# Performance work log

Measured on AMD Instinct MI355X. Metric: run time of the kernel, lower is better.

The kernel has to match this reference:

```python
import jax, jax.numpy as jnp
import numpy as np

B, P, ENC = 32, 196, 2048
E, H, A, V, T = 512, 512, 512, 10000, 21
S = 0.02  # param init scale


def setup_inputs() -> dict:
    key = jax.random.key(0)
    ks = jax.random.split(key, 10)
    return {
        "encoder_out": jax.random.normal(ks[0], (B, P, ENC), jnp.float32),
        "captions": jax.random.randint(ks[1], (B, T), 0, V),
        "emb": jax.random.normal(ks[2], (V, E), jnp.float32) * S,
        "enc_W": jax.random.normal(ks[3], (A, ENC), jnp.float32) * S,
        "enc_b": jnp.zeros((A,), jnp.float32),
        "dec_W": jax.random.normal(ks[4], (A, H), jnp.float32) * S,
        "dec_b": jnp.zeros((A,), jnp.float32),
        "att_W": jax.random.normal(ks[5], (1, A), jnp.float32) * S,
        "att_b": jnp.zeros((1,), jnp.float32),
        "W_ih": jax.random.normal(ks[6], (4 * H, E + ENC), jnp.float32) * S,
        "W_hh": jax.random.normal(ks[7], (4 * H, H), jnp.float32) * S,
        "b_ih": jnp.zeros((4 * H,), jnp.float32),
        "b_hh": jnp.zeros((4 * H,), jnp.float32),
        "fc_W": jax.random.normal(ks[8], (V, H), jnp.float32) * S,
        "fc_b": jnp.zeros((V,), jnp.float32),
    }


def reference(encoder_out, captions, emb, enc_W, enc_b, dec_W, dec_b,
              att_W, att_b, W_ih, W_hh, b_ih, b_hh, fc_W, fc_b):
    # teacher-forced embeddings: [B, T-1, E]
    embeddings = emb[captions[:, :-1]]
    # encoder projection is hidden-independent -> hoist out of the loop (same math)
    enc_proj = jnp.einsum('bpd,ad->bpa', encoder_out, enc_W) + enc_b  # [B,P,A]

    h0 = jnp.zeros((encoder_out.shape[0], H), encoder_out.dtype)
    c0 = jnp.zeros_like(h0)

    def step(carry, x_t):  # x_t: [B,E]
        h, c = carry
        dec_proj = h @ dec_W.T + dec_b                              # [B,A]
        e = jnp.tanh(enc_proj + dec_proj[:, None, :])               # [B,P,A]
        att = jnp.einsum('bpa,a->bp', e, att_W[0]) + att_b[0]       # [B,P]
        alpha = jax.nn.softmax(att, axis=1)
        context = jnp.einsum('bp,bpd->bd', alpha, encoder_out)      # [B,ENC]
        inp = jnp.concatenate([x_t, context], axis=1)               # [B,E+ENC]
        gates = inp @ W_ih.T + b_ih + h @ W_hh.T + b_hh             # [B,4H]
        i, f, g, o = jnp.split(gates, 4, axis=1)
        c2 = jax.nn.sigmoid(f) * c + jax.nn.sigmoid(i) * jnp.tanh(g)
        h2 = jax.nn.sigmoid(o) * jnp.tanh(c2)
        logits = h2 @ fc_W.T + fc_b                                 # [B,V]
        return (h2, c2), logits

    xs = jnp.swapaxes(embeddings, 0, 1)                             # [T-1,B,E]
    _, outs = jax.lax.scan(step, (h0, c0), xs)                      # [T-1,B,V]
    return jnp.swapaxes(outs, 0, 1)                                 # [B,T-1,V]
```

## Files before the change

kernel.cpp:

```cpp
#include <hip/hip_runtime.h>
#include <math.h>

typedef unsigned short u16;
typedef __attribute__((ext_vector_type(8))) short bf8;
typedef __attribute__((ext_vector_type(8))) unsigned short u16x8;
typedef __attribute__((ext_vector_type(4))) float f32x4;

constexpr int NB = 32;
constexpr int NP = 196;
constexpr int NE = 2048;
constexpr int ED = 512;
constexpr int HH = 512;
constexpr int AA = 512;
constexpr int NV = 10000;
constexpr int NT = 20;

__device__ inline u16 f2bf(float f) {
    unsigned u = __builtin_bit_cast(unsigned, f);
    u += 0x7fffu + ((u >> 16) & 1u);
    return (u16)(u >> 16);
}
__device__ inline float bf2f(u16 h) {
    return __builtin_bit_cast(float, (unsigned)h << 16);
}
__device__ inline void cvt8(const float* __restrict__ s, u16* __restrict__ d) {
    float4 v0 = *(const float4*)s, v1 = *(const float4*)(s + 4);
    u16x8 o;
    o[0] = f2bf(v0.x); o[1] = f2bf(v0.y); o[2] = f2bf(v0.z); o[3] = f2bf(v0.w);
    o[4] = f2bf(v1.x); o[5] = f2bf(v1.y); o[6] = f2bf(v1.z); o[7] = f2bf(v1.w);
    *(u16x8*)d = o;
}

__device__ inline void gld16(const u16* g, u16* l) {
    __builtin_amdgcn_global_load_lds(
        (const __attribute__((address_space(1))) void*)g,
        (__attribute__((address_space(3))) void*)l, 16, 0, 0);
}

__global__ void k_convert(const float* __restrict__ enc, const float* __restrict__ enc_W,
                          const float* __restrict__ dec_W, const float* __restrict__ W_ih,
                          const float* __restrict__ W_hh, const float* __restrict__ fc_W,
                          const float* __restrict__ emb, const int* __restrict__ caps,
                          u16* __restrict__ Xbf, u16* __restrict__ Wencbf,
                          u16* __restrict__ decWbf, u16* __restrict__ Wihbf,
                          u16* __restrict__ Whhbf, u16* __restrict__ fcWbf,
                          u16* __restrict__ embg, float* __restrict__ cbuf,
                          u16* __restrict__ hbf) {
    long g = (long)blockIdx.x * 256 + threadIdx.x;
    if (g < 1605632) { cvt8(enc + g * 8, Xbf + g * 8); return; }
    g -= 1605632;
    if (g < 131072) { cvt8(enc_W + g * 8, Wencbf + g * 8); return; }
    g -= 131072;
    if (g < 32768) { cvt8(dec_W + g * 8, decWbf + g * 8); return; }
    g -= 32768;
    if (g < 655360) { cvt8(W_ih + g * 8, Wihbf + g * 8); return; }
    g -= 655360;
    if (g < 131072) { cvt8(W_hh + g * 8, Whhbf + g * 8); return; }
    g -= 131072;
    if (g < 640000) { cvt8(fc_W + g * 8, fcWbf + g * 8); return; }
    g -= 640000;
    if (g < 40960) {
        long w = g >> 6, e8 = (g & 63) * 8;
        long b = w / 20, t = w - b * 20;
        int tok = caps[b * 21 + t];
        cvt8(emb + (size_t)tok * 512 + e8, embg + (size_t)w * 512 + e8);
        return;
    }
    g -= 40960;
    if (g < 2048) {
        *(float4*)(cbuf + g * 8) = make_float4(0.f, 0.f, 0.f, 0.f);
        *(float4*)(cbuf + g * 8 + 4) = make_float4(0.f, 0.f, 0.f, 0.f);
        return;
    }
    g -= 2048;
    if (g < 2048) { u16x8 z = {}; *(u16x8*)(hbf + g * 8) = z; }
}

__global__ __launch_bounds__(256) void k_encxw(const u16* __restrict__ Xbf,
                                               const u16* __restrict__ Wencbf,
                                               const u16* __restrict__ Wihbf,
                                               const float* __restrict__ enc_b,
                                               float* __restrict__ encproj,
                                               u16* __restrict__ XWbf) {
    __shared__ u16 As[2][128 * 32];
    __shared__ u16 Bs[2][128 * 32];
    int tid = threadIdx.x, lane = tid & 63, w = tid >> 6;
    int wr = w >> 1, wc = w & 1;
    int i0 = blockIdx.x * 128, j0 = blockIdx.y * 128;
    int ar = lane & 15, kg = lane >> 4;

    int srow = tid >> 2;
    int sc = (tid & 3) * 8;
    const u16* gA0 = Xbf + (size_t)(i0 + srow) * NE + sc;
    const u16* gA1 = gA0 + (size_t)64 * NE;
    size_t bstr;
    const u16* gB0;
    if (j0 < 512) { bstr = 2048; gB0 = Wencbf + (size_t)(j0 + srow) * 2048 + sc; }
    else          { bstr = 2560; gB0 = Wihbf + (size_t)(j0 - 512 + srow) * 2560 + 512 + sc; }
    const u16* gB1 = gB0 + 64 * bstr;

    f32x4 acc[4][4] = {};

#define STAGE_EX(buf, k0)                                   \
    do {                                                    \
        gld16(gA0 + (k0), &As[buf][tid * 8]);               \
        gld16(gA1 + (k0), &As[buf][2048 + tid * 8]);        \
        gld16(gB0 + (k0), &Bs[buf][tid * 8]);               \
        gld16(gB1 + (k0), &Bs[buf][2048 + tid * 8]);        \
    } while (0)

    STAGE_EX(0, 0);
    __syncthreads();
    for (int ks = 0; ks < 64; ++ks) {
        int cur = ks & 1;
        if (ks < 63) STAGE_EX(cur ^ 1, (ks + 1) * 32);
        bf8 a[4], b[4];
#pragma unroll
        for (int m = 0; m < 4; ++m)
            a[m] = *(const bf8*)(&As[cur][(wr * 64 + m * 16 + ar) * 32 + kg * 8]);
#pragma unroll
        for (int n = 0; n < 4; ++n)
            b[n] = *(const bf8*)(&Bs[cur][(wc * 64 + n * 16 + ar) * 32 + kg * 8]);
#pragma unroll
        for (int m = 0; m < 4; ++m)
#pragma unroll
            for (int n = 0; n < 4; ++n)
                acc[m][n] = __builtin_amdgcn_mfma_f32_16x16x32_bf16(a[m], b[n], acc[m][n], 0, 0, 0);
        if (ks < 63) __syncthreads();
    }
#undef STAGE_EX

    int rbase = kg * 4;
    if (j0 < 512) {
#pragma unroll
        for (int m = 0; m < 4; ++m) {
            int row = i0 + wr * 64 + m * 16 + rbase;
#pragma unroll
            for (int n = 0; n < 4; ++n) {
                int col = j0 + wc * 64 + n * 16 + ar;
                float bias = enc_b[col];
#pragma unroll
                for (int r = 0; r < 4; ++r)
                    encproj[(size_t)(row + r) * AA + col] = acc[m][n][r] + bias;
            }
        }
    } else {
#pragma unroll
        for (int m = 0; m < 4; ++m) {
            int row = i0 + wr * 64 + m * 16 + rbase;
#pragma unroll
            for (int n = 0; n < 4; ++n) {
                int col = j0 - 512 + wc * 64 + n * 16 + ar;
#pragma unroll
                for (int r = 0; r < 4; ++r)
                    XWbf[(size_t)(row + r) * 2048 + col] = f2bf(acc[m][n][r]);
            }
        }
    }
}

__global__ __launch_bounds__(256) void k_gpre(const u16* __restrict__ embg,
                                              const u16* __restrict__ Wihbf,
                                              float* __restrict__ gpre) {
    __shared__ u16 As[2][64 * 32];
    __shared__ u16 Bs[2][128 * 32];
    int tid = threadIdx.x, lane = tid & 63, w = tid >> 6;
    int wr = w >> 1, wc = w & 1;
    int i0 = blockIdx.x * 64, j0 = blockIdx.y * 128;
    int ar = lane & 15, kg = lane >> 4;

    int srow = tid >> 2;
    int sc = (tid & 3) * 8;
    const u16* gA  = embg + (size_t)(i0 + srow) * 512 + sc;
    const u16* gB0 = Wihbf + (size_t)(j0 + srow) * 2560 + sc;
    const u16* gB1 = Wihbf + (size_t)(j0 + 64 + srow) * 2560 + sc;

    f32x4 acc[2][4] = {};

#define STAGE_GP(buf, k0)                                   \
    do {                                                    \
        gld16(gA + (k0), &As[buf][tid * 8]);                \
        gld16(gB0 + (k0), &Bs[buf][tid * 8]);               \
        gld16(gB1 + (k0), &Bs[buf][2048 + tid * 8]);        \
    } while (0)

    STAGE_GP(0, 0);
    __syncthreads();
    for (int ks = 0; ks < 16; ++ks) {
        int cur = ks & 1;
        if (ks < 15) STAGE_GP(cur ^ 1, (ks + 1) * 32);
        bf8 a[2], b[4];
#pragma unroll
        for (int m = 0; m < 2; ++m)
            a[m] = *(const bf8*)(&As[cur][(wr * 32 + m * 16 + ar) * 32 + kg * 8]);
#pragma unroll
        for (int n = 0; n < 4; ++n)
            b[n] = *(const bf8*)(&Bs[cur][(wc * 64 + n * 16 + ar) * 32 + kg * 8]);
#pragma unroll
        for (int m = 0; m < 2; ++m)
#pragma unroll
            for (int n = 0; n < 4; ++n)
                acc[m][n] = __builtin_amdgcn_mfma_f32_16x16x32_bf16(a[m], b[n], acc[m][n], 0, 0, 0);
        if (ks < 15) __syncthreads();
    }
#undef STAGE_GP

    int rbase = kg * 4;
#pragma unroll
    for (int m = 0; m < 2; ++m) {
        int row = i0 + wr * 32 + m * 16 + rbase;
#pragma unroll
        for (int n = 0; n < 4; ++n) {
            int col = j0 + wc * 64 + n * 16 + ar;
#pragma unroll
            for (int r = 0; r < 4; ++r)
                gpre[(size_t)(row + r) * 2048 + col] = acc[m][n][r];
        }
    }
}

__global__ __launch_bounds__(256) void k_hproj(const u16* __restrict__ hbf,
                                               const u16* __restrict__ decWbf,
                                               const u16* __restrict__ Whhbf,
                                               float* __restrict__ dpart,
                                               float* __restrict__ ghh) {
    int tid = threadIdx.x, lane = tid & 63;
    int ww = blockIdx.x * 4 + (tid >> 6);
    int ar = lane & 15, kg = lane >> 4, koff = kg * 8;
    if (ww < 64) {
        int ks = ww >> 4, rem = ww & 15, rg = rem >> 3, cg = rem & 7;
        const u16* Arow = hbf + (rg * 16 + ar) * HH + koff + ks * 128;
        f32x4 acc[4] = {};
#pragma unroll
        for (int s = 0; s < 4; ++s) {
            int k0 = s * 32;
            bf8 a = *(const bf8*)(Arow + k0);
#pragma unroll
            for (int jt = 0; jt < 4; ++jt) {
                bf8 b = *(const bf8*)(decWbf + (cg * 64 + jt * 16 + ar) * HH + ks * 128 + k0 + koff);
                acc[jt] = __builtin_amdgcn_mfma_f32_16x16x32_bf16(a, b, acc[jt], 0, 0, 0);
            }
        }
        int bb = rg * 16 + kg * 4;
#pragma unroll
        for (int jt = 0; jt < 4; ++jt) {
            int col = cg * 64 + jt * 16 + ar;
#pragma unroll
            for (int r = 0; r < 4; ++r)
                dpart[(ks * NB + bb + r) * AA + col] = acc[jt][r];
        }
    } else {
        int q = ww - 64;
        int ks2 = q >> 6, rem = q & 63, cg = rem & 31, rg = rem >> 5;
        const u16* Arow = hbf + (rg * 16 + ar) * HH + ks2 * 128 + koff;
        f32x4 acc[4] = {};
#pragma unroll
        for (int s = 0; s < 4; ++s) {
            int k0 = s * 32;
            bf8 a = *(const bf8*)(Arow + k0);
#pragma unroll
            for (int jt = 0; jt < 4; ++jt) {
                int c = cg * 64 + jt * 16 + ar;
                bf8 b = *(const bf8*)(Whhbf + (size_t)c * HH + ks2 * 128 + k0 + koff);
                acc[jt] = __builtin_amdgcn_mfma_f32_16x16x32_bf16(a, b, acc[jt], 0, 0, 0);
            }
        }
        int bb = rg * 16 + kg * 4;
#pragma unroll
        for (int jt = 0; jt < 4; ++jt) {
            int col = cg * 64 + jt * 16 + ar;
#pragma unroll
            for (int r = 0; r < 4; ++r)
                ghh[(size_t)(ks2 * NB + bb + r) * 2048 + col] = acc[jt][r];
        }
    }
}

__global__ __launch_bounds__(256) void k_attexp(const float* __restrict__ encproj,
                                                const float* __restrict__ dpart,
                                                const float* __restrict__ dec_b,
                                                const float* __restrict__ att_W,
                                                const float* __restrict__ att_b,
                                                float* __restrict__ attb) {
    int tid = threadIdx.x, lane = tid & 63;
    int row = blockIdx.x * 4 + (tid >> 6);
    int b = row / NP;
    const f32x4* ep = (const f32x4*)(encproj + (size_t)row * AA);
    const f32x4* d0 = (const f32x4*)(dpart + b * AA);
    const f32x4* d1 = (const f32x4*)(dpart + (NB + b) * AA);
    const f32x4* d2 = (const f32x4*)(dpart + (2 * NB + b) * AA);
    const f32x4* d3 = (const f32x4*)(dpart + (3 * NB + b) * AA);
    const f32x4* db = (const f32x4*)dec_b;
    const f32x4* aw = (const f32x4*)att_W;
    float s = 0.f;
#pragma unroll
    for (int h = 0; h < 2; ++h) {
        int ix = h * 64 + lane;
        f32x4 x = ep[ix];
        f32x4 d = d0[ix] + d1[ix] + d2[ix] + d3[ix] + db[ix];
        f32x4 wv = aw[ix];
        s += tanhf(x[0] + d[0]) * wv[0] + tanhf(x[1] + d[1]) * wv[1] +
             tanhf(x[2] + d[2]) * wv[2] + tanhf(x[3] + d[3]) * wv[3];
    }
#pragma unroll
    for (int off = 32; off > 0; off >>= 1) s += __shfl_down(s, off, 64);
    if (lane == 0) attb[row] = expf(s + att_b[0]);
}

__global__ __launch_bounds__(512) void k_ctxg(const float* __restrict__ attb,
                                              const u16* __restrict__ XWbf,
                                              float* __restrict__ gctx) {
    int b = blockIdx.x >> 4, chunk = blockIdx.x & 15;
    int tid = threadIdx.x;
    __shared__ float sa[NP];
    __shared__ float sred[4][128];
    __shared__ float ssum;
    if (tid < NP) sa[tid] = attb[b * NP + tid];
    __syncthreads();
    if (tid < 64) {
        float s = 0.f;
        for (int p = tid; p < NP; p += 64) s += sa[p];
#pragma unroll
        for (int off = 32; off > 0; off >>= 1) s += __shfl_down(s, off, 64);
        if (tid == 0) ssum = s;
    }
    __syncthreads();
    float inv = 1.f / ssum;
    int col_l = tid & 127, pg = tid >> 7;
    int col = chunk * 128 + col_l;
    const u16* e = XWbf + (size_t)(b * NP + pg * 49) * 2048 + col;
    float acc = 0.f;
#pragma unroll 7
    for (int p = 0; p < 49; ++p) acc += sa[pg * 49 + p] * bf2f(e[(size_t)p * 2048]);
    sred[pg][col_l] = acc;
    __syncthreads();
    if (tid < 128) {
        float v = (sred[0][tid] + sred[1][tid] + sred[2][tid] + sred[3][tid]) * inv;
        gctx[(size_t)b * 2048 + chunk * 128 + tid] = v;
    }
}

__global__ void k_cell(const float* __restrict__ gpre, const float* __restrict__ ghh,
                       const float* __restrict__ gctx, const float* __restrict__ b_ih,
                       const float* __restrict__ b_hh, float* __restrict__ cbuf,
                       u16* __restrict__ hbf, u16* __restrict__ hallbf, int t) {
    int idx = blockIdx.x * 256 + threadIdx.x;
    int b = idx >> 9, j = idx & 511;
    float g4[4];
#pragma unroll
    for (int q = 0; q < 4; ++q) {
        int col = j + q * 512;
        float s = b_ih[col] + b_hh[col]
                + gpre[((size_t)b * 20 + t) * 2048 + col]
                + gctx[(size_t)b * 2048 + col];
#pragma unroll
        for (int ks = 0; ks < 4; ++ks) s += ghh[(size_t)(ks * NB + b) * 2048 + col];
        g4[q] = s;
    }
    float si = 1.f / (1.f + expf(-g4[0]));
    float sf = 1.f / (1.f + expf(-g4[1]));
    float so = 1.f / (1.f + expf(-g4[3]));
    float c2 = sf * cbuf[idx] + si * tanhf(g4[2]);
    cbuf[idx] = c2;
    u16 hb = f2bf(so * tanhf(c2));
    hbf[b * 512 + j] = hb;
    hallbf[(b * 20 + t) * 512 + j] = hb;
}

__global__ __launch_bounds__(256) void k_logits(const u16* __restrict__ hallbf,
                                                const u16* __restrict__ fcWbf,
                                                const float* __restrict__ fc_b,
                                                float* __restrict__ out) {
    __shared__ u16 As[2][128 * 32];
    __shared__ u16 Bs[2][128 * 32];
    int tid = threadIdx.x, lane = tid & 63, w = tid >> 6;
    int wr = w >> 1, wc = w & 1;
    int i0 = blockIdx.x * 128, j0 = blockIdx.y * 128;
    int ar = lane & 15, kg = lane >> 4;

    int srow = tid >> 2;
    int sc = (tid & 3) * 8;
    int brow0 = min(j0 + srow, NV - 1);
    int brow1 = min(j0 + 64 + srow, NV - 1);
    const u16* gA0 = hallbf + (size_t)(i0 + srow) * HH + sc;
    const u16* gA1 = hallbf + (size_t)(i0 + 64 + srow) * HH + sc;
    const u16* gB0 = fcWbf + (size_t)brow0 * HH + sc;
    const u16* gB1 = fcWbf + (size_t)brow1 * HH + sc;

    f32x4 acc[4][4] = {};

#define STAGE_LG(buf, k0)                                   \
    do {                                                    \
        gld16(gA0 + (k0), &As[buf][tid * 8]);               \
        gld16(gA1 + (k0), &As[buf][2048 + tid * 8]);        \
        gld16(gB0 + (k0), &Bs[buf][tid * 8]);               \
        gld16(gB1 + (k0), &Bs[buf][2048 + tid * 8]);        \
    } while (0)

    STAGE_LG(0, 0);
    __syncthreads();
    for (int ks = 0; ks < 16; ++ks) {
        int cur = ks & 1;
        if (ks < 15) STAGE_LG(cur ^ 1, (ks + 1) * 32);
        bf8 a[4], b[4];
#pragma unroll
        for (int m = 0; m < 4; ++m)
            a[m] = *(const bf8*)(&As[cur][(wr * 64 + m * 16 + ar) * 32 + kg * 8]);
#pragma unroll
        for (int n = 0; n < 4; ++n)
            b[n] = *(const bf8*)(&Bs[cur][(wc * 64 + n * 16 + ar) * 32 + kg * 8]);
#pragma unroll
        for (int m = 0; m < 4; ++m)
#pragma unroll
            for (int n = 0; n < 4; ++n)
                acc[m][n] = __builtin_amdgcn_mfma_f32_16x16x32_bf16(a[m], b[n], acc[m][n], 0, 0, 0);
        if (ks < 15) __syncthreads();
    }
#undef STAGE_LG

    int rbase = kg * 4;
#pragma unroll
    for (int m = 0; m < 4; ++m) {
        int row = i0 + wr * 64 + m * 16 + rbase;
#pragma unroll
        for (int n = 0; n < 4; ++n) {
            int col = j0 + wc * 64 + n * 16 + ar;
            if (col < NV) {
                float bias = fc_b[col];
#pragma unroll
                for (int r = 0; r < 4; ++r)
                    out[(size_t)(row + r) * NV + col] = acc[m][n][r] + bias;
            }
        }
    }
}

extern "C" void kernel_launch(void* const* d_in, const int* in_sizes, int n_in,
                              void* d_out, int out_size, void* d_ws, size_t ws_size,
                              hipStream_t stream) {
    (void)in_sizes; (void)n_in; (void)out_size; (void)ws_size;
    const float* enc   = (const float*)d_in[0];
    const int*   caps  = (const int*)d_in[1];
    const float* emb   = (const float*)d_in[2];
    const float* enc_W = (const float*)d_in[3];
    const float* enc_b = (const float*)d_in[4];
    const float* dec_W = (const float*)d_in[5];
    const float* dec_b = (const float*)d_in[6];
    const float* att_W = (const float*)d_in[7];
    const float* att_b = (const float*)d_in[8];
    const float* W_ih  = (const float*)d_in[9];
    const float* W_hh  = (const float*)d_in[10];
    const float* b_ih  = (const float*)d_in[11];
    const float* b_hh  = (const float*)d_in[12];
    const float* fc_W  = (const float*)d_in[13];
    const float* fc_b  = (const float*)d_in[14];
    float* out = (float*)d_out;

    char* base = (char*)d_ws;
    float* encproj = (float*)base;                 base += (size_t)6272 * 512 * 4;
    float* dpart   = (float*)base;                 base += (size_t)4 * 32 * 512 * 4;
    float* attb    = (float*)base;                 base += (size_t)6272 * 4;
    float* cbuf    = (float*)base;                 base += (size_t)32 * 512 * 4;
    float* ghh     = (float*)base;                 base += (size_t)4 * 32 * 2048 * 4;
    float* gctx    = (float*)base;                 base += (size_t)32 * 2048 * 4;
    float* gpre    = (float*)base;                 base += (size_t)640 * 2048 * 4;
    u16* Xbf    = (u16*)base;                      base += (size_t)32 * 196 * 2048 * 2;
    u16* Wencbf = (u16*)base;                      base += (size_t)512 * 2048 * 2;
    u16* decWbf = (u16*)base;                      base += (size_t)512 * 512 * 2;
    u16* Wihbf  = (u16*)base;                      base += (size_t)2048 * 2560 * 2;
    u16* Whhbf  = (u16*)base;                      base += (size_t)2048 * 512 * 2;
    u16* fcWbf  = (u16*)base;                      base += (size_t)10000 * 512 * 2;
    u16* embg   = (u16*)base;                      base += (size_t)32 * 20 * 512 * 2;
    u16* XWbf   = (u16*)base;                      base += (size_t)6272 * 2048 * 2;
    u16* hbf    = (u16*)base;                      base += (size_t)32 * 512 * 2;
    u16* hallbf = (u16*)base;                      base += (size_t)32 * 20 * 512 * 2;

    k_convert<<<12660, 256, 0, stream>>>(enc, enc_W, dec_W, W_ih, W_hh, fc_W, emb, caps,
                                         Xbf, Wencbf, decWbf, Wihbf, Whhbf, fcWbf,
                                         embg, cbuf, hbf);
    k_encxw<<<dim3(49, 20), 256, 0, stream>>>(Xbf, Wencbf, Wihbf, enc_b, encproj, XWbf);
    k_gpre<<<dim3(10, 16), 256, 0, stream>>>(embg, Wihbf, gpre);
    for (int t = 0; t < NT; ++t) {
        k_hproj<<<80, 256, 0, stream>>>(hbf, decWbf, Whhbf, dpart, ghh);
        k_attexp<<<1568, 256, 0, stream>>>(encproj, dpart, dec_b, att_W, att_b, attb);
        k_ctxg<<<512, 512, 0, stream>>>(attb, XWbf, gctx);
        k_cell<<<64, 256, 0, stream>>>(gpre, ghh, gctx, b_ih, b_hh, cbuf, hbf,
                                       hallbf, t);
    }
    k_logits<<<dim3(5, 79), 256, 0, stream>>>(hallbf, fcWbf, fc_b, out);
}
```

Measured before the change: 539.4 us.

## Fuse context reduction with LSTM cell, store encoder projection in bf16, remap blocks across XCDs

The context-weighted gate reduction and the LSTM cell update are merged into one kernel. Each block now covers 32 hidden units across all four gates, so the gctx buffer and one launch per timestep go away. The encoder projection is stored as bf16 instead of fp32, which halves the bytes k_attexp reads on every step at some cost in attention precision. The encoder GEMM also remaps block IDs so neighbouring tiles land on the same XCD for better L2 locality.

Measured after the change: 571.1 us. 1.06x slower.

```diff
diff --git a/kernel.cpp b/kernel.cpp
--- a/kernel.cpp
+++ b/kernel.cpp
@@ -80,13 +80,18 @@
                                                const u16* __restrict__ Wencbf,
                                                const u16* __restrict__ Wihbf,
                                                const float* __restrict__ enc_b,
-                                               float* __restrict__ encproj,
+                                               u16* __restrict__ encprojbf,
                                                u16* __restrict__ XWbf) {
     __shared__ u16 As[2][128 * 32];
     __shared__ u16 Bs[2][128 * 32];
     int tid = threadIdx.x, lane = tid & 63, w = tid >> 6;
     int wr = w >> 1, wc = w & 1;
-    int i0 = blockIdx.x * 128, j0 = blockIdx.y * 128;
+
+    int old = blockIdx.y * 49 + blockIdx.x;
+    int xcd = old & 7, off = old >> 3;
+    int nid = (xcd < 4 ? xcd * 123 : 492 + (xcd - 4) * 122) + off;
+    int i0 = (nid / 20) * 128, j0 = (nid % 20) * 128;
+
     int ar = lane & 15, kg = lane >> 4;
 
     int srow = tid >> 2;
@@ -141,7 +146,7 @@
                 float bias = enc_b[col];
 #pragma unroll
                 for (int r = 0; r < 4; ++r)
-                    encproj[(size_t)(row + r) * AA + col] = acc[m][n][r] + bias;
+                    encprojbf[(size_t)(row + r) * AA + col] = f2bf(acc[m][n][r] + bias);
             }
         }
     } else {
@@ -276,7 +281,7 @@
     }
 }
 
-__global__ __launch_bounds__(256) void k_attexp(const float* __restrict__ encproj,
+__global__ __launch_bounds__(256) void k_attexp(const u16* __restrict__ encprojbf,
                                                 const float* __restrict__ dpart,
                                                 const float* __restrict__ dec_b,
                                                 const float* __restrict__ att_W,
@@ -285,32 +290,37 @@
     int tid = threadIdx.x, lane = tid & 63;
     int row = blockIdx.x * 4 + (tid >> 6);
     int b = row / NP;
-    const f32x4* ep = (const f32x4*)(encproj + (size_t)row * AA);
+    bf8 x = *(const bf8*)(encprojbf + (size_t)row * AA + lane * 8);
     const f32x4* d0 = (const f32x4*)(dpart + b * AA);
     const f32x4* d1 = (const f32x4*)(dpart + (NB + b) * AA);
     const f32x4* d2 = (const f32x4*)(dpart + (2 * NB + b) * AA);
     const f32x4* d3 = (const f32x4*)(dpart + (3 * NB + b) * AA);
     const f32x4* db = (const f32x4*)dec_b;
     const f32x4* aw = (const f32x4*)att_W;
+    int ixA = lane * 2, ixB = lane * 2 + 1;
+    f32x4 dA = d0[ixA] + d1[ixA] + d2[ixA] + d3[ixA] + db[ixA];
+    f32x4 dB = d0[ixB] + d1[ixB] + d2[ixB] + d3[ixB] + db[ixB];
+    f32x4 wA = aw[ixA], wB = aw[ixB];
     float s = 0.f;
 #pragma unroll
-    for (int h = 0; h < 2; ++h) {
-        int ix = h * 64 + lane;
-        f32x4 x = ep[ix];
-        f32x4 d = d0[ix] + d1[ix] + d2[ix] + d3[ix] + db[ix];
-        f32x4 wv = aw[ix];
-        s += tanhf(x[0] + d[0]) * wv[0] + tanhf(x[1] + d[1]) * wv[1] +
-             tanhf(x[2] + d[2]) * wv[2] + tanhf(x[3] + d[3]) * wv[3];
-    }
+    for (int q = 0; q < 4; ++q) s += tanhf(bf2f((u16)x[q]) + dA[q]) * wA[q];
+#pragma unroll
+    for (int q = 0; q < 4; ++q) s += tanhf(bf2f((u16)x[4 + q]) + dB[q]) * wB[q];
 #pragma unroll
     for (int off = 32; off > 0; off >>= 1) s += __shfl_down(s, off, 64);
     if (lane == 0) attb[row] = expf(s + att_b[0]);
 }
 
-__global__ __launch_bounds__(512) void k_ctxg(const float* __restrict__ attb,
-                                              const u16* __restrict__ XWbf,
-                                              float* __restrict__ gctx) {
-    int b = blockIdx.x >> 4, chunk = blockIdx.x & 15;
+__global__ __launch_bounds__(512) void k_ctxgcell(const float* __restrict__ attb,
+                                                  const u16* __restrict__ XWbf,
+                                                  const float* __restrict__ gpre,
+                                                  const float* __restrict__ ghh,
+                                                  const float* __restrict__ b_ih,
+                                                  const float* __restrict__ b_hh,
+                                                  float* __restrict__ cbuf,
+                                                  u16* __restrict__ hbf,
+                                                  u16* __restrict__ hallbf, int t) {
+    int b = blockIdx.x >> 4, ch = blockIdx.x & 15;
     int tid = threadIdx.x;
     __shared__ float sa[NP];
     __shared__ float sred[4][128];
@@ -326,45 +336,38 @@
     }
     __syncthreads();
     float inv = 1.f / ssum;
-    int col_l = tid & 127, pg = tid >> 7;
-    int col = chunk * 128 + col_l;
-    const u16* e = XWbf + (size_t)(b * NP + pg * 49) * 2048 + col;
+    int l = tid & 127, pg = tid >> 7;
+    int gcol = (l >> 5) * 512 + ch * 32 + (l & 31);
+    const u16* e = XWbf + (size_t)(b * NP + pg * 49) * 2048 + gcol;
     float acc = 0.f;
 #pragma unroll 7
     for (int p = 0; p < 49; ++p) acc += sa[pg * 49 + p] * bf2f(e[(size_t)p * 2048]);
-    sred[pg][col_l] = acc;
-    __syncthreads();
-    if (tid < 128) {
-        float v = (sred[0][tid] + sred[1][tid] + sred[2][tid] + sred[3][tid]) * inv;
-        gctx[(size_t)b * 2048 + chunk * 128 + tid] = v;
-    }
-}
-
-__global__ void k_cell(const float* __restrict__ gpre, const float* __restrict__ ghh,
-                       const float* __restrict__ gctx, const float* __restrict__ b_ih,
-                       const float* __restrict__ b_hh, float* __restrict__ cbuf,
-                       u16* __restrict__ hbf, u16* __restrict__ hallbf, int t) {
-    int idx = blockIdx.x * 256 + threadIdx.x;
-    int b = idx >> 9, j = idx & 511;
-    float g4[4];
-#pragma unroll
-    for (int q = 0; q < 4; ++q) {
-        int col = j + q * 512;
-        float s = b_ih[col] + b_hh[col]
-                + gpre[((size_t)b * 20 + t) * 2048 + col]
-                + gctx[(size_t)b * 2048 + col];
-#pragma unroll
-        for (int ks = 0; ks < 4; ++ks) s += ghh[(size_t)(ks * NB + b) * 2048 + col];
-        g4[q] = s;
-    }
-    float si = 1.f / (1.f + expf(-g4[0]));
-    float sf = 1.f / (1.f + expf(-g4[1]));
-    float so = 1.f / (1.f + expf(-g4[3]));
-    float c2 = sf * cbuf[idx] + si * tanhf(g4[2]);
-    cbuf[idx] = c2;
-    u16 hb = f2bf(so * tanhf(c2));
-    hbf[b * 512 + j] = hb;
-    hallbf[(b * 20 + t) * 512 + j] = hb;
+    sred[pg][l] = acc;
+    __syncthreads();
+    if (tid < 128)
+        sred[0][tid] = (sred[0][tid] + sred[1][tid] + sred[2][tid] + sred[3][tid]) * inv;
+    __syncthreads();
+    if (tid < 32) {
+        int j = ch * 32 + tid;
+        float g4[4];
+#pragma unroll
+        for (int q = 0; q < 4; ++q) {
+            int gc = q * 512 + j;
+            float s = sred[0][q * 32 + tid] + b_ih[gc] + b_hh[gc]
+                    + gpre[((size_t)b * 20 + t) * 2048 + gc];
+#pragma unroll
+            for (int ks = 0; ks < 4; ++ks) s += ghh[(size_t)(ks * NB + b) * 2048 + gc];
+            g4[q] = s;
+        }
+        float si = 1.f / (1.f + expf(-g4[0]));
+        float sf = 1.f / (1.f + expf(-g4[1]));
+        float so = 1.f / (1.f + expf(-g4[3]));
+        float c2 = sf * cbuf[b * 512 + j] + si * tanhf(g4[2]);
+        cbuf[b * 512 + j] = c2;
+        u16 hb = f2bf(so * tanhf(c2));
+        hbf[b * 512 + j] = hb;
+        hallbf[(b * 20 + t) * 512 + j] = hb;
+    }
 }
 
 __global__ __launch_bounds__(256) void k_logits(const u16* __restrict__ hallbf,
@@ -457,13 +460,12 @@
     float* out = (float*)d_out;
 
     char* base = (char*)d_ws;
-    float* encproj = (float*)base;                 base += (size_t)6272 * 512 * 4;
     float* dpart   = (float*)base;                 base += (size_t)4 * 32 * 512 * 4;
     float* attb    = (float*)base;                 base += (size_t)6272 * 4;
     float* cbuf    = (float*)base;                 base += (size_t)32 * 512 * 4;
     float* ghh     = (float*)base;                 base += (size_t)4 * 32 * 2048 * 4;
-    float* gctx    = (float*)base;                 base += (size_t)32 * 2048 * 4;
     float* gpre    = (float*)base;                 base += (size_t)640 * 2048 * 4;
+    u16* encprojbf = (u16*)base;                   base += (size_t)6272 * 512 * 2;
     u16* Xbf    = (u16*)base;                      base += (size_t)32 * 196 * 2048 * 2;
     u16* Wencbf = (u16*)base;                      base += (size_t)512 * 2048 * 2;
     u16* decWbf = (u16*)base;                      base += (size_t)512 * 512 * 2;
@@ -478,14 +480,14 @@
     k_convert<<<12660, 256, 0, stream>>>(enc, enc_W, dec_W, W_ih, W_hh, fc_W, emb, caps,
                                          Xbf, Wencbf, decWbf, Wihbf, Whhbf, fcWbf,
                                          embg, cbuf, hbf);
-    k_encxw<<<dim3(49, 20), 256, 0, stream>>>(Xbf, Wencbf, Wihbf, enc_b, encproj, XWbf);
+    k_encxw<<<dim3(49, 20), 256, 0, stream>>>(Xbf, Wencbf, Wihbf, enc_b,
+                                              encprojbf, XWbf);
     k_gpre<<<dim3(10, 16), 256, 0, stream>>>(embg, Wihbf, gpre);
     for (int t = 0; t < NT; ++t) {
         k_hproj<<<80, 256, 0, stream>>>(hbf, decWbf, Whhbf, dpart, ghh);
-        k_attexp<<<1568, 256, 0, stream>>>(encproj, dpart, dec_b, att_W, att_b, attb);
-        k_ctxg<<<512, 512, 0, stream>>>(attb, XWbf, gctx);
-        k_cell<<<64, 256, 0, stream>>>(gpre, ghh, gctx, b_ih, b_hh, cbuf, hbf,
-                                       hallbf, t);
+        k_attexp<<<1568, 256, 0, stream>>>(encprojbf, dpart, dec_b, att_W, att_b, attb);
+        k_ctxgcell<<<512, 512, 0, stream>>>(attb, XWbf, gpre, ghh, b_ih, b_hh,
+                                            cbuf, hbf, hallbf, t);
     }
     k_logits<<<dim3(5, 79), 256, 0, stream>>>(hallbf, fcWbf, fc_b, out);
 }
```
